# Kernel optimization log

Measured on AMD Instinct MI355X. Metric: run time of the kernel, lower is better.

The kernel has to match this reference:

```python
import jax, jax.numpy as jnp
import numpy as np

T, B, E = 1024, 4, 1024
H = 16
D = E // H          # head_dim = 64
L = 16              # max_relative_length


def setup_inputs() -> dict:
    key = jax.random.key(0)
    ks = jax.random.split(key, 4)
    query = jax.random.normal(ks[0], (T, B, E), dtype=jnp.float32)
    # xavier-ish scaled params
    in_proj_weight = jax.random.normal(ks[1], (3 * E, E), dtype=jnp.float32) * (1.0 / np.sqrt(E))
    in_proj_bias = jnp.zeros((3 * E,), dtype=jnp.float32)
    rel_pos_keys = jax.random.normal(ks[2], (2 * L + 1, E), dtype=jnp.float32) * (1.0 / np.sqrt(E))
    out_w = jax.random.normal(ks[3], (E, E), dtype=jnp.float32) * (1.0 / np.sqrt(E))
    out_b = jnp.zeros((E,), dtype=jnp.float32)
    return {"query": query, "in_proj_weight": in_proj_weight, "in_proj_bias": in_proj_bias,
            "rel_pos_keys": rel_pos_keys, "out_w": out_w, "out_b": out_b}


def reference(query, in_proj_weight, in_proj_bias, rel_pos_keys, out_w, out_b):
    t, b, e = query.shape
    scaling = D ** (-0.5)
    # fused qkv projection: [T,B,3E]
    qkv = jnp.einsum('tbe,fe->tbf', query, in_proj_weight) + in_proj_bias
    q, k, v = jnp.split(qkv, 3, axis=-1)
    q = q * scaling
    # [T,B,E] -> [B*H, T, D]
    def heads(x):
        return x.reshape(t, b * H, D).transpose(1, 0, 2)
    q, k, v = heads(q), heads(k), heads(v)
    # clipped relative position matrix [T,T] in [0, 2L]
    r = jnp.arange(t)
    dist = jnp.clip(r[None, :] - r[:, None], -L, L) + L
    # gather relation keys, keep first head_dim channels: [T,T,D]
    rel_k = rel_pos_keys[dist][:, :, :D]
    # scores = q k^T + q . rel_k  (Shaw et al.), [B*H, T, T]
    scores = jnp.einsum('btd,bsd->bts', q, k) + jnp.einsum('btd,tsd->bts', q, rel_k)
    probs = jax.nn.softmax(scores, axis=-1)
    attn = jnp.einsum('bts,bsd->btd', probs, v)      # [B*H, T, D]
    attn = attn.transpose(1, 0, 2).reshape(t, b, e)   # [T, B, E]
    return jnp.einsum('tbe,oe->tbo', attn, out_w) + out_b
```

## Files before the change

### kernel.cpp

```cpp
#include <hip/hip_runtime.h>
#include <hip/hip_bf16.h>

typedef __attribute__((ext_vector_type(8))) short short8;
typedef __attribute__((ext_vector_type(4))) float floatx4;


#define QSCALE 0.18033688011112043f

__device__ __forceinline__ short f2bf(float x) {
  union { float f; unsigned u; } cv; cv.f = x;
  unsigned u = cv.u + (0x7FFFu + ((cv.u >> 16) & 1u));
  return (short)(u >> 16);
}

__device__ __forceinline__ unsigned pk_bf16(float a, float b) {
  union { __hip_bfloat162 h; unsigned u; } cv;
  cv.h = __float22bfloat162_rn(make_float2(a, b));
  return cv.u;
}

__device__ __forceinline__ float exp2_hw(float x) {
  return __builtin_amdgcn_exp2f(x);
}

__device__ __forceinline__ floatx4 mfma16(short8 a, short8 b, floatx4 c) {
  return __builtin_amdgcn_mfma_f32_16x16x32_bf16(a, b, c, 0, 0, 0);
}

__device__ __forceinline__ void async_copy16(const void* g, void* l) {
  __builtin_amdgcn_global_load_lds((const __attribute__((address_space(1))) void*)g,
                                   (__attribute__((address_space(3))) void*)l, 16, 0, 0);
}

__global__ void __launch_bounds__(256) convert_all_kernel(
    const float* __restrict__ s0, const float* __restrict__ s1,
    const float* __restrict__ s2,
    short* __restrict__ d0, short* __restrict__ d1, short* __restrict__ d2)
{
  int i = blockIdx.x * 256 + threadIdx.x;
  if (i < 524288) {
    int e8 = i & 127, b = (i >> 7) & 3, t = i >> 9;
    const float4* s = (const float4*)s0 + (size_t)i * 2;
    float4 a = s[0], c = s[1];
    uint4 o = make_uint4(pk_bf16(a.x, a.y), pk_bf16(a.z, a.w),
                         pk_bf16(c.x, c.y), pk_bf16(c.z, c.w));
    *(uint4*)(d0 + (size_t)b * 1048576 + t * 1024 + e8 * 8) = o;
  } else {
    const float* src; short* dst; int off;
    if (i < 917504) { src = s1; dst = d1; off = i - 524288; }
    else            { src = s2; dst = d2; off = i - 917504; }
    const float4* s = (const float4*)src + (size_t)off * 2;
    float4 a = s[0], c = s[1];
    uint4 o = make_uint4(pk_bf16(a.x, a.y), pk_bf16(a.z, a.w),
                         pk_bf16(c.x, c.y), pk_bf16(c.z, c.w));
    *(uint4*)(dst + (size_t)off * 8) = o;
  }
}

__global__ void __launch_bounds__(512, 2) gemm_qkv(
    const short* __restrict__ A, const short* __restrict__ W,
    const float* __restrict__ bias,
    short* __restrict__ q_ws, short* __restrict__ k_ws, short* __restrict__ v_ws)
{
  __shared__ __align__(16) short Atile[2 * 256 * 64];
  __shared__ __align__(16) short Btile[2 * 192 * 64];
  const int tid = threadIdx.x, lane = tid & 63, w = tid >> 6;
  const int quad = lane >> 4, l16 = lane & 15;
  const int m0 = blockIdx.x * 256, n0 = blockIdx.y * 192;
  const int wmh = (w >> 2);
  const int wn = (w & 3) * 48;

  const short* Ag = A + (size_t)m0 * 1024;
  const short* Wg = W + (size_t)n0 * 1024;

  floatx4 acc[8][3];
  #pragma unroll
  for (int mt = 0; mt < 8; mt++)
    #pragma unroll
    for (int nt = 0; nt < 3; nt++) acc[mt][nt] = (floatx4)(0.0f);

  #define STAGE_A(kc, buf)                                                   \
    {                                                                        \
      _Pragma("unroll")                                                      \
      for (int i = 0; i < 4; i++) {                                          \
        int seg = i * 512 + tid;                                             \
        int row = seg >> 3, p = seg & 7;                                     \
        int ck = p ^ (row & 7);                                              \
        async_copy16(Ag + (size_t)row * 1024 + (kc) * 64 + ck * 8,           \
                     Atile + (buf) * 16384 + (size_t)(i * 512 + w * 64) * 8);\
      }                                                                      \
    }
  #define STAGE_B(kc, buf)                                                   \
    {                                                                        \
      _Pragma("unroll")                                                      \
      for (int i = 0; i < 3; i++) {                                          \
        int seg = i * 512 + tid;                                             \
        int row = seg >> 3, p = seg & 7;                                     \
        int ck = p ^ (row & 7);                                              \
        async_copy16(Wg + (size_t)row * 1024 + (kc) * 64 + ck * 8,           \
                     Btile + (buf) * 12288 + (size_t)(i * 512 + w * 64) * 8);\
      }                                                                      \
    }

  STAGE_A(0, 0); STAGE_B(0, 0);
  asm volatile("s_waitcnt vmcnt(0)" ::: "memory");
  __builtin_amdgcn_s_barrier();

  for (int kt = 0; kt < 16; ++kt) {
    const int cur = kt & 1, nxt = cur ^ 1;
    const int kc1 = (kt + 1 < 16) ? kt + 1 : 15;

    short8 af[8][2], bf[3][2];
    #pragma unroll
    for (int mt = 0; mt < 8; mt++) {
      int r = mt * 16 + l16;
      int gr = wmh * 128 + r;
      #pragma unroll
      for (int ks = 0; ks < 2; ks++)
        af[mt][ks] = *(const short8*)(Atile + cur * 16384 + gr * 64
                                      + (((quad + 4 * ks) ^ (r & 7)) << 3));
    }
    #pragma unroll
    for (int nt = 0; nt < 3; nt++) {
      int row = wn + nt * 16 + l16;
      #pragma unroll
      for (int ks = 0; ks < 2; ks++)
        bf[nt][ks] = *(const short8*)(Btile + cur * 12288 + row * 64
                                      + (((quad + 4 * ks) ^ (row & 7)) << 3));
    }

    STAGE_A(kc1, nxt); STAGE_B(kc1, nxt);

    __builtin_amdgcn_s_setprio(1);
    #pragma unroll
    for (int mt = 0; mt < 8; mt++)
      #pragma unroll
      for (int nt = 0; nt < 3; nt++)
        #pragma unroll
        for (int ks = 0; ks < 2; ks++)
          acc[mt][nt] = mfma16(af[mt][ks], bf[nt][ks], acc[mt][nt]);
    __builtin_amdgcn_s_setprio(0);
    __builtin_amdgcn_sched_barrier(0);

    asm volatile("s_waitcnt vmcnt(0)" ::: "memory");
    __builtin_amdgcn_s_barrier();
  }
  #undef STAGE_A
  #undef STAGE_B

  #pragma unroll
  for (int nt = 0; nt < 3; nt++) {
    int f = n0 + wn + nt * 16 + l16;
    float bv = bias[f];
    int which = f >> 10;
    int h = (f >> 6) & 15;
    int d = f & 63;
    if (which == 2) {
      #pragma unroll
      for (int mt = 0; mt < 8; mt++) {
        int r0 = m0 + wmh * 128 + mt * 16 + quad * 4;
        int t = r0 & 1023, bb = r0 >> 10;
        int bh = bb * 16 + h;
        unsigned lo = pk_bf16(acc[mt][nt][0] + bv, acc[mt][nt][1] + bv);
        unsigned hi = pk_bf16(acc[mt][nt][2] + bv, acc[mt][nt][3] + bv);
        *(uint2*)(v_ws + ((size_t)bh * 64 + d) * 1024 + t) = make_uint2(lo, hi);
      }
    } else {
      short* dst = which ? k_ws : q_ws;
      const float sc = which ? 1.0f : QSCALE;
      #pragma unroll
      for (int mt = 0; mt < 8; mt++) {
        int r0 = m0 + wmh * 128 + mt * 16 + quad * 4;
        int t = r0 & 1023, bb = r0 >> 10;
        int bh = bb * 16 + h;
        unsigned u01 = pk_bf16((acc[mt][nt][0] + bv) * sc, (acc[mt][nt][1] + bv) * sc);
        unsigned u23 = pk_bf16((acc[mt][nt][2] + bv) * sc, (acc[mt][nt][3] + bv) * sc);
        size_t base = ((size_t)bh * 1024 + t) * 64 + d;
        dst[base]           = (short)u01;
        dst[base + 64]      = (short)(u01 >> 16);
        dst[base + 128]     = (short)u23;
        dst[base + 192]     = (short)(u23 >> 16);
      }
    }
  }
}

__global__ void __launch_bounds__(256) attn_kernel(
    const short* __restrict__ q_ws, const short* __restrict__ k_ws,
    const short* __restrict__ v_ws, const float* __restrict__ relk,
    short* __restrict__ attn_ws)
{
  __shared__ float rel_lds[128 * 33];
  __shared__ __align__(16) short Ktile[2][64 * 64];
  __shared__ __align__(16) short Vtile[2][64 * 64];
  __shared__ __align__(16) short p_lds[4][32 * 64];
  const int tid = threadIdx.x, lane = tid & 63, w = tid >> 6;
  const int quad = lane >> 4, l16 = lane & 15;
  const int bh = 8 * ((int)blockIdx.x & 7) + (((int)blockIdx.x >> 3) & 7);
  const int t0 = ((int)blockIdx.x >> 6) * 128;
  const int b = bh >> 4, h = bh & 15;

  short8 aq[2][2];
  #pragma unroll
  for (int qt = 0; qt < 2; qt++)
    #pragma unroll
    for (int ks = 0; ks < 2; ks++)
      aq[qt][ks] = *(const short8*)(q_ws
          + ((size_t)bh * 1024 + t0 + qt * 64 + w * 16 + l16) * 64
          + ks * 32 + quad * 8);

  for (int i = tid; i < 48 * 8; i += 256) {
    int row = i >> 3, p = i & 7;
    short8 val;
    if (row < 33) {
      const float* src = relk + row * 1024 + p * 8;
      float4 a = *(const float4*)src, c = *(const float4*)(src + 4);
      val[0] = f2bf(a.x); val[1] = f2bf(a.y); val[2] = f2bf(a.z); val[3] = f2bf(a.w);
      val[4] = f2bf(c.x); val[5] = f2bf(c.y); val[6] = f2bf(c.z); val[7] = f2bf(c.w);
    } else {
      val = (short8)0;
    }
    *(short8*)(Ktile[0] + row * 64 + ((p ^ (row & 7)) << 3)) = val;
  }
  __syncthreads();

  #pragma unroll
  for (int qt = 0; qt < 2; qt++) {
    #pragma unroll
    for (int jt = 0; jt < 3; jt++) {
      floatx4 scR = (floatx4)(0.0f);
      #pragma unroll
      for (int ks = 0; ks < 2; ks++) {
        int rrow = jt * 16 + l16;
        int ck = (quad + 4 * ks) ^ (rrow & 7);
        short8 rb = *(const short8*)(Ktile[0] + rrow * 64 + ck * 8);
        scR = mfma16(aq[qt][ks], rb, scR);
      }
      int j = jt * 16 + l16;
      if (j < 33) {
        #pragma unroll
        for (int reg = 0; reg < 4; reg++) {
          int tl = qt * 64 + w * 16 + quad * 4 + reg;
          rel_lds[tl * 33 + j] = scR[reg];
        }
      }
    }
  }
  __syncthreads();

  float biasLo[2], biasHi[2];
  #pragma unroll
  for (int qt = 0; qt < 2; qt++) {
    int ql = qt * 64 + w * 16 + l16;
    biasLo[qt] = rel_lds[ql * 33 + 0];
    biasHi[qt] = rel_lds[ql * 33 + 32];
  }

  floatx4 o[2][4];
  #pragma unroll
  for (int qt = 0; qt < 2; qt++)
    #pragma unroll
    for (int dt = 0; dt < 4; dt++) o[qt][dt] = (floatx4)(0.0f);
  float rsum[2] = {0.f, 0.f};

  const short* kg = k_ws + (size_t)bh * 1024 * 64;
  const short* vg = v_ws + (size_t)bh * 64 * 1024;

  #define STAGE_KV(S0, BUF)                                                  \
    {                                                                        \
      _Pragma("unroll")                                                      \
      for (int i = 0; i < 2; i++) {                                          \
        int seg = i * 256 + tid;                                             \
        int row = seg >> 3, p = seg & 7;                                     \
        int ck = p ^ (row & 7);                                              \
        async_copy16(kg + (size_t)((S0) + row) * 64 + ck * 8,                \
                     Ktile[BUF] + (size_t)(i * 256 + w * 64) * 8);           \
        async_copy16(vg + (size_t)row * 1024 + (S0) + ck * 8,                \
                     Vtile[BUF] + (size_t)(i * 256 + w * 64) * 8);           \
      }                                                                      \
    }

  STAGE_KV(0, 0);

  for (int st = 0; st < 16; st++) {
    const int s0 = st * 64;
    const int cur = st & 1;
    __syncthreads();
    if (st < 15) STAGE_KV(s0 + 64, 1 - cur);

    short8 kb[4][2];
    #pragma unroll
    for (int nt = 0; nt < 4; nt++)
      #pragma unroll
      for (int ks = 0; ks < 2; ks++) {
        int srow = nt * 16 + l16;
        kb[nt][ks] = *(const short8*)(Ktile[cur] + srow * 64
                                      + (((quad + 4 * ks) ^ (l16 & 7)) << 3));
      }

    floatx4 sc[2][4];
    __builtin_amdgcn_s_setprio(1);
    #pragma unroll
    for (int qt = 0; qt < 2; qt++)
      #pragma unroll
      for (int nt = 0; nt < 4; nt++) {
        sc[qt][nt] = (floatx4)(0.0f);
        #pragma unroll
        for (int ks = 0; ks < 2; ks++)
          sc[qt][nt] = mfma16(kb[nt][ks], aq[qt][ks], sc[qt][nt]);
      }
    __builtin_amdgcn_s_setprio(0);

    #pragma unroll
    for (int qt = 0; qt < 2; qt++) {
      const int qbase = t0 + qt * 64 + w * 16;
      bool alllo = (s0 <= qbase - 79);
      bool allhi = (s0 >= qbase + 31);
      if (alllo || allhi) {
        float bb = alllo ? biasLo[qt] : biasHi[qt];
        #pragma unroll
        for (int nt = 0; nt < 4; nt++)
          #pragma unroll
          for (int reg = 0; reg < 4; reg++) sc[qt][nt][reg] += bb;
      } else {
        int ql = qt * 64 + w * 16 + l16;
        #pragma unroll
        for (int nt = 0; nt < 4; nt++)
          #pragma unroll
          for (int reg = 0; reg < 4; reg++) {
            int delta = (s0 + 16 * nt + 4 * quad + reg) - (qbase + l16);
            delta = min(max(delta, -16), 16) + 16;
            sc[qt][nt][reg] += rel_lds[ql * 33 + delta];
          }
      }
      #pragma unroll
      for (int nt = 0; nt < 4; nt++) {
        #pragma unroll
        for (int reg = 0; reg < 4; reg++) {
          float p = exp2_hw(sc[qt][nt][reg]);
          sc[qt][nt][reg] = p;
          rsum[qt] += p;
        }
        unsigned w0 = pk_bf16(sc[qt][nt][0], sc[qt][nt][1]);
        unsigned w1 = pk_bf16(sc[qt][nt][2], sc[qt][nt][3]);
        int srot = (16 * nt + 4 * quad + 4 * l16) & 63;
        *(uint2*)(p_lds[w] + (qt * 16 + l16) * 64 + srot) = make_uint2(w0, w1);
      }
    }

    short8 ap[2][2];
    #pragma unroll
    for (int qt = 0; qt < 2; qt++)
      #pragma unroll
      for (int ks = 0; ks < 2; ks++) {
        int s1 = (32 * ks + 8 * quad + 4 * l16) & 63;
        int s2 = (s1 + 4) & 63;
        union { short8 v; uint2 u[2]; } pu;
        pu.u[0] = *(const uint2*)(p_lds[w] + (qt * 16 + l16) * 64 + s1);
        pu.u[1] = *(const uint2*)(p_lds[w] + (qt * 16 + l16) * 64 + s2);
        ap[qt][ks] = pu.v;
      }

    __builtin_amdgcn_s_setprio(1);
    #pragma unroll
    for (int dt = 0; dt < 4; dt++) {
      short8 vb[2];
      #pragma unroll
      for (int ks = 0; ks < 2; ks++) {
        int drow = dt * 16 + l16;
        vb[ks] = *(const short8*)(Vtile[cur] + drow * 64
                                  + (((quad + 4 * ks) ^ (l16 & 7)) << 3));
      }
      #pragma unroll
      for (int qt = 0; qt < 2; qt++)
        #pragma unroll
        for (int ks = 0; ks < 2; ks++)
          o[qt][dt] = mfma16(ap[qt][ks], vb[ks], o[qt][dt]);
    }
    __builtin_amdgcn_s_setprio(0);
  }
  #undef STAGE_KV

  #pragma unroll
  for (int qt = 0; qt < 2; qt++) {
    float rs = rsum[qt];
    rs += __shfl_xor(rs, 16, 64);
    rs += __shfl_xor(rs, 32, 64);
    float inv[4];
    #pragma unroll
    for (int reg = 0; reg < 4; reg++)
      inv[reg] = 1.0f / __shfl(rs, quad * 4 + reg, 64);
    #pragma unroll
    for (int dt = 0; dt < 4; dt++) {
      unsigned u01 = pk_bf16(o[qt][dt][0] * inv[0], o[qt][dt][1] * inv[1]);
      unsigned u23 = pk_bf16(o[qt][dt][2] * inv[2], o[qt][dt][3] * inv[3]);
      int tg = t0 + qt * 64 + w * 16 + quad * 4;
      size_t base = ((size_t)tg * 4 + b) * 1024 + h * 64 + dt * 16 + l16;
      attn_ws[base]         = (short)u01;
      attn_ws[base + 4096]  = (short)(u01 >> 16);
      attn_ws[base + 8192]  = (short)u23;
      attn_ws[base + 12288] = (short)(u23 >> 16);
    }
  }
}

__global__ void __launch_bounds__(256) gemm_outproj(
    const short* __restrict__ A, const short* __restrict__ W,
    const float* __restrict__ bias, float* __restrict__ out)
{
  __shared__ __align__(16) short Atile[2 * 64 * 32];
  __shared__ __align__(16) short Btile[2 * 128 * 32];
  const int tid = threadIdx.x;
  const int m0 = blockIdx.x * 64, n0 = blockIdx.y * 128;
  const int lane = tid & 63, w = tid >> 6;
  const int quad = lane >> 4, l16 = lane & 15;
  const int wm = (w >> 1) * 32, wn = (w & 1) * 64;

  floatx4 acc[2][4];
  #pragma unroll
  for (int mt = 0; mt < 2; mt++)
    #pragma unroll
    for (int nt = 0; nt < 4; nt++) acc[mt][nt] = (floatx4)(0.0f);

  #define STAGE_OP(KK, BUF)                                                  \
    {                                                                        \
      _Pragma("unroll")                                                      \
      for (int i = 0; i < 2; i++) {                                          \
        int seg = i * 256 + tid;                \
        int row = seg >> 2, p = seg & 3;                                     \
        int ck = (p - ((row >> 1) & 3)) & 3;                                 \
        async_copy16(W + (size_t)(n0 + row) * 1024 + (KK) + ck * 8,          \
                     Btile + (size_t)((BUF) * 4096 + (i * 256 + w * 64) * 8)); \
      }                                                                      \
      {                                                                      \
        int row = tid >> 2, p = tid & 3;         \
        int ck = (p - ((row >> 1) & 3)) & 3;                                 \
        async_copy16(A + (size_t)(m0 + row) * 1024 + (KK) + ck * 8,          \
                     Atile + (size_t)((BUF) * 2048 + (w * 64) * 8));         \
      }                                                                      \
    }

  STAGE_OP(0, 0);
  for (int kk = 0; kk < 1024; kk += 32) {
    const int cur = (kk >> 5) & 1;
    const short* Ac = Atile + cur * 2048;
    const short* Bc = Btile + cur * 4096;
    __syncthreads();
    if (kk + 32 < 1024) STAGE_OP(kk + 32, 1 - cur);
    short8 af[2], bfr[4];
    #pragma unroll
    for (int mt = 0; mt < 2; mt++) {
      int R = wm + mt * 16 + l16;
      af[mt] = *(const short8*)(Ac + R * 32 + ((quad + (R >> 1)) & 3) * 8);
    }
    #pragma unroll
    for (int nt = 0; nt < 4; nt++) {
      int R = wn + nt * 16 + l16;
      bfr[nt] = *(const short8*)(Bc + R * 32 + ((quad + (R >> 1)) & 3) * 8);
    }
    #pragma unroll
    for (int mt = 0; mt < 2; mt++)
      #pragma unroll
      for (int nt = 0; nt < 4; nt++)
        acc[mt][nt] = mfma16(af[mt], bfr[nt], acc[mt][nt]);
  }
  #undef STAGE_OP

  #pragma unroll
  for (int nt = 0; nt < 4; nt++) {
    int f = n0 + wn + nt * 16 + l16;
    float bv = bias[f];
    #pragma unroll
    for (int mt = 0; mt < 2; mt++) {
      #pragma unroll
      for (int reg = 0; reg < 4; reg++) {
        int r = m0 + wm + mt * 16 + quad * 4 + reg;
        out[(size_t)r * 1024 + f] = acc[mt][nt][reg] + bv;
      }
    }
  }
}

extern "C" void kernel_launch(void* const* d_in, const int* in_sizes, int n_in,
                              void* d_out, int out_size, void* d_ws, size_t ws_size,
                              hipStream_t stream) {
  const float* query = (const float*)d_in[0];
  const float* in_w  = (const float*)d_in[1];
  const float* in_b  = (const float*)d_in[2];
  const float* relk  = (const float*)d_in[3];
  const float* out_w = (const float*)d_in[4];
  const float* out_b = (const float*)d_in[5];
  float* out = (float*)d_out;

  short* qry_bf = (short*)d_ws;
  short* win_bf = qry_bf + (size_t)4096 * 1024;
  short* wout_bf = win_bf + (size_t)3072 * 1024;
  short* q_ws   = wout_bf + (size_t)1024 * 1024;
  short* k_ws   = q_ws + (size_t)64 * 1024 * 64;
  short* v_ws   = k_ws + (size_t)64 * 1024 * 64;
  short* att_ws = v_ws + (size_t)64 * 1024 * 64;

  convert_all_kernel<<<4096, 256, 0, stream>>>(query, in_w, out_w,
                                               qry_bf, win_bf, wout_bf);
  gemm_qkv<<<dim3(16, 16), 512, 0, stream>>>(qry_bf, win_bf, in_b, q_ws, k_ws, v_ws);
  attn_kernel<<<512, 256, 0, stream>>>(q_ws, k_ws, v_ws, relk, att_ws);
  gemm_outproj<<<dim3(64, 8), 256, 0, stream>>>(att_ws, wout_bf, out_b, out);
}
```

Before: 168.3 us.

## Retile output projection GEMM to 128x128 with 64-wide K and XOR swizzle

The output-projection GEMM moves from 64x128 tiles with 256 threads and K-step 32 to 128x128 tiles with 512 threads and K-step 64. It reuses the QKV GEMM's XOR-swizzled async staging and its prio/barrier pipeline. Separately, in the QKV GEMM the prefetch of the next K tile is issued before the LDS fragment reads instead of after. The aim is more reuse per tile, fewer barriers, and earlier prefetch issue, at the cost of fewer blocks (256) for the out-projection and possibly lower occupancy.

```diff
diff --git a/kernel.cpp b/kernel.cpp
--- a/kernel.cpp
+++ b/kernel.cpp
@@ -110,6 +110,8 @@
     const int cur = kt & 1, nxt = cur ^ 1;
     const int kc1 = (kt + 1 < 16) ? kt + 1 : 15;
 
+    STAGE_A(kc1, nxt); STAGE_B(kc1, nxt);
+
     short8 af[8][2], bf[3][2];
     #pragma unroll
     for (int mt = 0; mt < 8; mt++) {
@@ -128,8 +130,6 @@
         bf[nt][ks] = *(const short8*)(Btile + cur * 12288 + row * 64
                                       + (((quad + 4 * ks) ^ (row & 7)) << 3));
     }
-
-    STAGE_A(kc1, nxt); STAGE_B(kc1, nxt);
 
     __builtin_amdgcn_s_setprio(1);
     #pragma unroll
@@ -404,77 +404,94 @@
   }
 }
 
-__global__ void __launch_bounds__(256) gemm_outproj(
+__global__ void __launch_bounds__(512, 2) gemm_outproj(
     const short* __restrict__ A, const short* __restrict__ W,
     const float* __restrict__ bias, float* __restrict__ out)
 {
-  __shared__ __align__(16) short Atile[2 * 64 * 32];
-  __shared__ __align__(16) short Btile[2 * 128 * 32];
-  const int tid = threadIdx.x;
-  const int m0 = blockIdx.x * 64, n0 = blockIdx.y * 128;
-  const int lane = tid & 63, w = tid >> 6;
+  __shared__ __align__(16) short Atile[2 * 128 * 64];
+  __shared__ __align__(16) short Btile[2 * 128 * 64];
+  const int tid = threadIdx.x, lane = tid & 63, w = tid >> 6;
   const int quad = lane >> 4, l16 = lane & 15;
-  const int wm = (w >> 1) * 32, wn = (w & 1) * 64;
-
-  floatx4 acc[2][4];
-  #pragma unroll
-  for (int mt = 0; mt < 2; mt++)
-    #pragma unroll
-    for (int nt = 0; nt < 4; nt++) acc[mt][nt] = (floatx4)(0.0f);
-
-  #define STAGE_OP(KK, BUF)                                                  \
+  const int m0 = blockIdx.x * 128, n0 = blockIdx.y * 128;
+  const int wmh = (w >> 2);
+  const int wn = (w & 3) * 32;
+
+  const short* Ag = A + (size_t)m0 * 1024;
+  const short* Wg = W + (size_t)n0 * 1024;
+
+  floatx4 acc[4][2];
+  #pragma unroll
+  for (int mt = 0; mt < 4; mt++)
+    #pragma unroll
+    for (int nt = 0; nt < 2; nt++) acc[mt][nt] = (floatx4)(0.0f);
+
+  #define STAGE_OP(kc, buf)                                                  \
     {                                                                        \
       _Pragma("unroll")                                                      \
       for (int i = 0; i < 2; i++) {                                          \
-        int seg = i * 256 + tid;                \
-        int row = seg >> 2, p = seg & 3;                                     \
-        int ck = (p - ((row >> 1) & 3)) & 3;                                 \
-        async_copy16(W + (size_t)(n0 + row) * 1024 + (KK) + ck * 8,          \
-                     Btile + (size_t)((BUF) * 4096 + (i * 256 + w * 64) * 8)); \
+        int seg = i * 512 + tid;                                             \
+        int row = seg >> 3, p = seg & 7;                                     \
+        int ck = p ^ (row & 7);                                              \
+        async_copy16(Ag + (size_t)row * 1024 + (kc) * 64 + ck * 8,           \
+                     Atile + (buf) * 8192 + (size_t)(i * 512 + w * 64) * 8); \
+        async_copy16(Wg + (size_t)row * 1024 + (kc) * 64 + ck * 8,           \
+                     Btile + (buf) * 8192 + (size_t)(i * 512 + w * 64) * 8); \
       }                                                                      \
-      {                                                                      \
-        int row = tid >> 2, p = tid & 3;         \
-        int ck = (p - ((row >> 1) & 3)) & 3;                                 \
-        async_copy16(A + (size_t)(m0 + row) * 1024 + (KK) + ck * 8,          \
-                     Atile + (size_t)((BUF) * 2048 + (w * 64) * 8));         \
-      }                                                                      \
     }
 
   STAGE_OP(0, 0);
-  for (int kk = 0; kk < 1024; kk += 32) {
-    const int cur = (kk >> 5) & 1;
-    const short* Ac = Atile + cur * 2048;
-    const short* Bc = Btile + cur * 4096;
-    __syncthreads();
-    if (kk + 32 < 1024) STAGE_OP(kk + 32, 1 - cur);
-    short8 af[2], bfr[4];
-    #pragma unroll
-    for (int mt = 0; mt < 2; mt++) {
-      int R = wm + mt * 16 + l16;
-      af[mt] = *(const short8*)(Ac + R * 32 + ((quad + (R >> 1)) & 3) * 8);
-    }
-    #pragma unroll
-    for (int nt = 0; nt < 4; nt++) {
-      int R = wn + nt * 16 + l16;
-      bfr[nt] = *(const short8*)(Bc + R * 32 + ((quad + (R >> 1)) & 3) * 8);
-    }
-    #pragma unroll
-    for (int mt = 0; mt < 2; mt++)
-      #pragma unroll
-      for (int nt = 0; nt < 4; nt++)
-        acc[mt][nt] = mfma16(af[mt], bfr[nt], acc[mt][nt]);
+  asm volatile("s_waitcnt vmcnt(0)" ::: "memory");
+  __builtin_amdgcn_s_barrier();
+
+  for (int kt = 0; kt < 16; ++kt) {
+    const int cur = kt & 1, nxt = cur ^ 1;
+    const int kc1 = (kt + 1 < 16) ? kt + 1 : 15;
+
+    STAGE_OP(kc1, nxt);
+
+    short8 af[4][2], bf[2][2];
+    #pragma unroll
+    for (int mt = 0; mt < 4; mt++) {
+      int gr = wmh * 64 + mt * 16 + l16;
+      #pragma unroll
+      for (int ks = 0; ks < 2; ks++)
+        af[mt][ks] = *(const short8*)(Atile + cur * 8192 + gr * 64
+                                      + (((quad + 4 * ks) ^ (gr & 7)) << 3));
+    }
+    #pragma unroll
+    for (int nt = 0; nt < 2; nt++) {
+      int row = wn + nt * 16 + l16;
+      #pragma unroll
+      for (int ks = 0; ks < 2; ks++)
+        bf[nt][ks] = *(const short8*)(Btile + cur * 8192 + row * 64
+                                      + (((quad + 4 * ks) ^ (row & 7)) << 3));
+    }
+
+    __builtin_amdgcn_s_setprio(1);
+    #pragma unroll
+    for (int mt = 0; mt < 4; mt++)
+      #pragma unroll
+      for (int nt = 0; nt < 2; nt++)
+        #pragma unroll
+        for (int ks = 0; ks < 2; ks++)
+          acc[mt][nt] = mfma16(af[mt][ks], bf[nt][ks], acc[mt][nt]);
+    __builtin_amdgcn_s_setprio(0);
+    __builtin_amdgcn_sched_barrier(0);
+
+    asm volatile("s_waitcnt vmcnt(0)" ::: "memory");
+    __builtin_amdgcn_s_barrier();
   }
   #undef STAGE_OP
 
   #pragma unroll
-  for (int nt = 0; nt < 4; nt++) {
+  for (int nt = 0; nt < 2; nt++) {
     int f = n0 + wn + nt * 16 + l16;
     float bv = bias[f];
     #pragma unroll
-    for (int mt = 0; mt < 2; mt++) {
+    for (int mt = 0; mt < 4; mt++) {
       #pragma unroll
       for (int reg = 0; reg < 4; reg++) {
-        int r = m0 + wm + mt * 16 + quad * 4 + reg;
+        int r = m0 + wmh * 64 + mt * 16 + quad * 4 + reg;
         out[(size_t)r * 1024 + f] = acc[mt][nt][reg] + bv;
       }
     }
@@ -504,5 +521,5 @@
                                                qry_bf, win_bf, wout_bf);
   gemm_qkv<<<dim3(16, 16), 512, 0, stream>>>(qry_bf, win_bf, in_b, q_ws, k_ws, v_ws);
   attn_kernel<<<512, 256, 0, stream>>>(q_ws, k_ws, v_ws, relk, att_ws);
-  gemm_outproj<<<dim3(64, 8), 256, 0, stream>>>(att_ws, wout_bf, out_b, out);
-}
+  gemm_outproj<<<dim3(32, 8), 512, 0, stream>>>(att_ws, wout_bf, out_b, out);
+}
```

Measured after the change: 172.6 us. 2.5% more time.
